# Kernel tuning notes

Measured on AMD Instinct MI355X. Metric: run time of the kernel, lower is better.

Reference implementation:

```python
import jax, jax.numpy as jnp
import numpy as np

B, N_PER, F_IN, HID, DEG = 64, 1024, 64, 128, 16
N = B * N_PER
E = N * DEG

def _ceil_k(k):
    return -((-4 * k) // 5)  # ceil(0.8 * k), static python int

def setup_inputs():
    key = jax.random.key(0)
    ks = jax.random.split(key, 16)
    x = jax.random.normal(ks[0], (N, F_IN), jnp.float32)
    # edges are intra-graph: local endpoints in [0, N_PER) offset by graph id
    loc = jax.random.randint(ks[1], (2, E), 0, N_PER, jnp.int32)
    gid = jnp.repeat(jnp.arange(B, dtype=jnp.int32), E // B)
    edge_index = loc + gid[None, :] * N_PER
    batch = jnp.repeat(jnp.arange(B, dtype=jnp.int32), N_PER)
    def lin(k, fi, fo):
        s = 1.0 / float(np.sqrt(fi))
        return jax.random.uniform(k, (fi, fo), jnp.float32, -s, s)
    inp = dict(x=x, edge_index=edge_index, batch=batch)
    inp["Wr1"] = lin(ks[2], F_IN, HID); inp["Wn1"] = lin(ks[3], F_IN, HID); inp["b1"] = jnp.zeros((HID,), jnp.float32)
    inp["Wr2"] = lin(ks[4], HID, HID); inp["Wn2"] = lin(ks[5], HID, HID); inp["b2"] = jnp.zeros((HID,), jnp.float32)
    inp["Wr3"] = lin(ks[6], HID, HID); inp["Wn3"] = lin(ks[7], HID, HID); inp["b3"] = jnp.zeros((HID,), jnp.float32)
    inp["p1"] = jax.random.normal(ks[8], (HID,), jnp.float32)
    inp["p2"] = jax.random.normal(ks[9], (HID,), jnp.float32)
    inp["p3"] = jax.random.normal(ks[10], (HID,), jnp.float32)
    inp["l1w"] = lin(ks[11], 2 * HID, HID); inp["l1b"] = jnp.zeros((HID,), jnp.float32)
    inp["l2w"] = lin(ks[12], HID, 2); inp["l2b"] = jnp.zeros((2,), jnp.float32)
    return inp

def _graph_conv(x, src, dst, emask, Wr, Wn, b, n_nodes):
    # x'_i = W1 x_i + sum_{j->i} W2 x_j + b ; masked edges contribute 0
    msg = x[src] * emask[:, None]                                  # [E, H]
    agg = jax.ops.segment_sum(msg, dst, num_segments=n_nodes)     # [N, H]
    return x @ Wr + agg @ Wn + b

def _topk_pool(x, src, dst, emask, p, k_prev):
    # PyG TopKPooling: score = x.p/||p||, keep ceil(0.8*n) per graph,
    # x_out = x[perm] * tanh(score[perm]); relabel+filter edges
    k_new = _ceil_k(k_prev)
    s = (x @ p) / jnp.linalg.norm(p)                               # [B*k_prev]
    vals, idx = jax.lax.top_k(s.reshape(B, k_prev), k_new)        # [B, k_new]
    perm = (idx + jnp.arange(B, dtype=idx.dtype)[:, None] * k_prev).reshape(-1)
    x_new = x[perm] * jnp.tanh(vals.reshape(-1))[:, None]
    inv = jnp.full((B * k_prev,), -1, jnp.int32).at[perm].set(jnp.arange(B * k_new, dtype=jnp.int32))
    ns, nd = inv[src], inv[dst]
    valid = emask * ((ns >= 0) & (nd >= 0)).astype(x.dtype)
    return x_new, jnp.maximum(ns, 0), jnp.maximum(nd, 0), valid, k_new

def _readout(x, k):
    b = jnp.repeat(jnp.arange(B, dtype=jnp.int32), k)
    gmax = jax.ops.segment_max(x, b, num_segments=B)
    gmean = jax.ops.segment_sum(x, b, num_segments=B) / k
    return jnp.concatenate([gmax, gmean], axis=1)                  # [B, 2H]

def reference(x, edge_index, batch, Wr1, Wn1, b1, Wr2, Wn2, b2, Wr3, Wn3, b3, p1, p2, p3, l1w, l1b, l2w, l2b):
    src, dst = edge_index[0], edge_index[1]
    emask = jnp.ones((E,), x.dtype)
    k = N_PER
    convs = [(Wr1, Wn1, b1), (Wr2, Wn2, b2), (Wr3, Wn3, b3)]
    pools = [p1, p2, p3]
    xs = []
    for (Wr, Wn, bb), p in zip(convs, pools):
        x = jax.nn.relu(_graph_conv(x, src, dst, emask, Wr, Wn, bb, B * k))
        x, src, dst, emask, k = _topk_pool(x, src, dst, emask, p, k)
        xs.append(_readout(x, k))
    h = xs[0] + xs[1] + xs[2]
    h = jax.nn.relu(h @ l1w + l1b)
    # F.dropout(p=0.5) skipped: eval-mode reference
    h = jax.nn.relu(h @ l2w + l2b)
    return jax.nn.log_softmax(h, axis=-1)
```

## Files before the change

kernel.cpp:

```cpp
#include <hip/hip_runtime.h>
#include <hip/hip_bf16.h>
#include <math.h>

#define NN   65536
#define NPER 1024
#define NE   1048576
#define NB   64

typedef __attribute__((ext_vector_type(8))) short short8;
typedef __attribute__((ext_vector_type(4))) float f32x4;


__global__ __launch_bounds__(256) void count_kernel(const int* __restrict__ ei, int* __restrict__ cnt){
  int e = blockIdx.x*256 + threadIdx.x;
  if (e < NE) atomicAdd(&cnt[ei[NE + e]], 1);
}

__global__ __launch_bounds__(1024) void scan1_kernel(const int* __restrict__ cnt,
      int* __restrict__ loc, int* __restrict__ bsum){
  __shared__ int wsum[16];
  int t = threadIdx.x;
  int i = blockIdx.x*1024 + t;
  int lane = t & 63, wid = t >> 6;
  int v = cnt[i];
  int s = v;
  #pragma unroll
  for (int d = 1; d < 64; d <<= 1){
    int src = (lane >= d) ? (lane - d) : lane;
    int u = __shfl(s, src);
    if (lane >= d) s += u;
  }
  if (lane == 63) wsum[wid] = s;
  __syncthreads();
  if (wid == 0){
    int ws = (lane < 16) ? wsum[lane] : 0;
    #pragma unroll
    for (int d = 1; d < 16; d <<= 1){
      int src = (lane >= d) ? (lane - d) : lane;
      int u = __shfl(ws, src);
      if (lane >= d) ws += u;
    }
    if (lane < 16) wsum[lane] = ws;
  }
  __syncthreads();
  int base = (wid > 0) ? wsum[wid - 1] : 0;
  loc[i] = base + s - v;
  if (t == 1023) bsum[blockIdx.x] = base + s;
}

__global__ __launch_bounds__(64) void scan2_kernel(const int* __restrict__ bsum, int* __restrict__ boff){
  int t = threadIdx.x;
  int v = bsum[t];
  int s = v;
  #pragma unroll
  for (int d = 1; d < 64; d <<= 1){
    int src = (t >= d) ? (t - d) : t;
    int u = __shfl(s, src);
    if (t >= d) s += u;
  }
  boff[t] = s - v;
}

__global__ __launch_bounds__(1024) void scan3_kernel(const int* __restrict__ loc, const int* __restrict__ boff,
      int* __restrict__ off, int* __restrict__ cursor){
  int i = blockIdx.x*1024 + threadIdx.x;
  int v = loc[i] + boff[blockIdx.x];
  off[i] = v;
  cursor[i] = v;
  if (i == NN - 1) off[NN] = NE;
}

__global__ __launch_bounds__(256) void fill_kernel(const int* __restrict__ ei, int* cursor, int* __restrict__ adj){
  int e = blockIdx.x*256 + threadIdx.x;
  if (e < NE){
    int pos = atomicAdd(&cursor[ei[NE + e]], 1);
    adj[pos] = ei[e];
  }
}


__global__ __launch_bounds__(256) void compact_kernel(const int* __restrict__ off, const int* __restrict__ adj,
      const float* __restrict__ scale, const int* __restrict__ alive,
      int* __restrict__ adj2, float* __restrict__ scl2, int* __restrict__ deg2){
  int w = (blockIdx.x*256 + (int)threadIdx.x) >> 6;
  int lane = threadIdx.x & 63;
  if (w >= NN) return;
  if (!alive[w]){ if (lane == 0) deg2[w] = 0; return; }
  int s0 = off[w], s1 = off[w+1];
  int base = s0;
  for (int e0 = s0; e0 < s1; e0 += 64){
    int e = e0 + lane;
    bool okE = e < s1;
    int s = adj[okE ? e : (s1 - 1)];
    float t = scale[s];
    bool keep = okE && (t != 0.f);
    unsigned long long m = __ballot(keep);
    int pos = base + __popcll(m & ((1ull << lane) - 1ull));
    if (keep){ adj2[pos] = s; scl2[pos] = t; }
    base += __popcll(m);
  }
  if (lane == 0) deg2[w] = base - s0;
}


__global__ __launch_bounds__(256) void gather_kernel(const float* __restrict__ x, int stride, int F,
      const int* __restrict__ off, const int* __restrict__ adj, const float* __restrict__ scl,
      const int* __restrict__ deg2, float* __restrict__ agg, const int* __restrict__ alive){
  int bid = blockIdx.x;
  bid = (bid & 7) * (gridDim.x >> 3) + (bid >> 3);
  int w = (bid*256 + (int)threadIdx.x) >> 6;
  int lane = threadIdx.x & 63;
  if (w >= NN) return;
  if (alive && !alive[w]) return;
  int s0 = off[w];
  int s1 = deg2 ? (s0 + deg2[w]) : off[w+1];
  if (F == 64){
    int sub = lane >> 4;
    int fl  = (lane & 15) * 4;
    float4 a0 = make_float4(0.f,0.f,0.f,0.f), a1 = a0;
    if (s1 > s0){
      for (int e = s0; e < s1; e += 8){
        int e0 = e + sub, e1 = e + 4 + sub;
        bool ok0 = e0 < s1, ok1 = e1 < s1;
        int sA = adj[ok0 ? e0 : (s1 - 1)];
        int sB = adj[ok1 ? e1 : (s1 - 1)];
        float t0 = ok0 ? 1.f : 0.f, t1 = ok1 ? 1.f : 0.f;
        float4 vA = *(const float4*)&x[(size_t)sA*stride + fl];
        float4 vB = *(const float4*)&x[(size_t)sB*stride + fl];
        a0.x = fmaf(vA.x, t0, a0.x); a0.y = fmaf(vA.y, t0, a0.y);
        a0.z = fmaf(vA.z, t0, a0.z); a0.w = fmaf(vA.w, t0, a0.w);
        a1.x = fmaf(vB.x, t1, a1.x); a1.y = fmaf(vB.y, t1, a1.y);
        a1.z = fmaf(vB.z, t1, a1.z); a1.w = fmaf(vB.w, t1, a1.w);
      }
    }
    a0.x += a1.x; a0.y += a1.y; a0.z += a1.z; a0.w += a1.w;
    #pragma unroll
    for (int m = 16; m <= 32; m <<= 1){
      a0.x += __shfl_xor(a0.x, m);
      a0.y += __shfl_xor(a0.y, m);
      a0.z += __shfl_xor(a0.z, m);
      a0.w += __shfl_xor(a0.w, m);
    }
    if (lane < 16) *(float4*)&agg[(size_t)w*128 + fl] = a0;
  } else {
    int sub = lane >> 5;
    int fl  = (lane & 31) * 4;
    float4 a[4];
    #pragma unroll
    for (int i = 0; i < 4; ++i) a[i] = make_float4(0.f,0.f,0.f,0.f);
    if (s1 > s0){
      for (int e = s0; e < s1; e += 8){
        int ss[4]; float tv[4];
        #pragma unroll
        for (int i = 0; i < 4; ++i){
          int ei = e + 2*i + sub;
          bool okE = ei < s1;
          int ii = okE ? ei : (s1 - 1);
          ss[i] = adj[ii];
          tv[i] = okE ? scl[ii] : 0.f;
        }
        #pragma unroll
        for (int i = 0; i < 4; ++i){
          float4 v = *(const float4*)&x[(size_t)ss[i]*stride + fl];
          a[i].x = fmaf(v.x, tv[i], a[i].x);
          a[i].y = fmaf(v.y, tv[i], a[i].y);
          a[i].z = fmaf(v.z, tv[i], a[i].z);
          a[i].w = fmaf(v.w, tv[i], a[i].w);
        }
      }
    }
    float4 r;
    r.x = (a[0].x + a[1].x) + (a[2].x + a[3].x);
    r.y = (a[0].y + a[1].y) + (a[2].y + a[3].y);
    r.z = (a[0].z + a[1].z) + (a[2].z + a[3].z);
    r.w = (a[0].w + a[1].w) + (a[2].w + a[3].w);
    r.x += __shfl_xor(r.x, 32);
    r.y += __shfl_xor(r.y, 32);
    r.z += __shfl_xor(r.z, 32);
    r.w += __shfl_xor(r.w, 32);
    if (lane < 32) *(float4*)&agg[(size_t)w*128 + fl] = r;
  }
}


__global__ __launch_bounds__(256) void wsplit_kernel(const float* __restrict__ Wr, const float* __restrict__ Wn,
      int Kx, int Kcat, unsigned short* __restrict__ WTh, unsigned short* __restrict__ WTl){
  int idx = blockIdx.x*256 + threadIdx.x;
  if (idx >= Kcat*128) return;
  int c = idx & 127, k = idx >> 7;
  float w = (k < Kx) ? Wr[k*128 + c] : Wn[(k - Kx)*128 + c];
  __hip_bfloat16 h = __float2bfloat16(w);
  float hf = __bfloat162float(h);
  __hip_bfloat16 l = __float2bfloat16(w - hf);
  WTh[(size_t)c*Kcat + k] = reinterpret_cast<unsigned short&>(h);
  WTl[(size_t)c*Kcat + k] = reinterpret_cast<unsigned short&>(l);
}


__global__ __launch_bounds__(256, 2) void conv_kernel(const float* __restrict__ xsrc, int strideX, int ntx,
      const float* aggb, int nta,
      const unsigned short* __restrict__ WTh, const unsigned short* __restrict__ WTl, int Kcat,
      const float* __restrict__ bias, const float* __restrict__ p, const float* __restrict__ scaleX,
      float* yout, float* __restrict__ score){
  __shared__ unsigned short XhL[128*32], XlL[128*32];
  __shared__ unsigned short WhL[128*32], WlL[128*32];
  __shared__ float sbuf[128*2];
  const int tid = threadIdx.x;
  const int row0 = blockIdx.x * 128;
  const int srow = tid & 127;
  const int shalf = tid >> 7;
  const int lane = tid & 63;
  const int wid = tid >> 6;
  const int wr = wid >> 1, wc = wid & 1;
  const int l15 = lane & 15, lkq = lane >> 4;

  const float xscale = scaleX ? scaleX[row0 + srow] : 1.f;

  f32x4 acc[4][4];
  #pragma unroll
  for (int m = 0; m < 4; ++m)
    #pragma unroll
    for (int j = 0; j < 4; ++j)
      acc[m][j] = (f32x4){0.f, 0.f, 0.f, 0.f};

  const int nt = ntx + nta;
  for (int t = 0; t < nt; ++t){
    __syncthreads();
    {
      const float* Xs   = (t < ntx) ? xsrc : aggb;
      const int stride  = (t < ntx) ? strideX : 128;
      const int kc      = (t < ntx) ? t*32 : (t - ntx)*32;
      const float sc    = (t < ntx) ? xscale : 1.f;
      #pragma unroll
      for (int kq2 = 0; kq2 < 2; ++kq2){
        const int kq = shalf*2 + kq2;
        const float* xp = Xs + (size_t)(row0 + srow)*stride + kc + kq*8;
        float4 v0 = *(const float4*)(xp);
        float4 v1 = *(const float4*)(xp + 4);
        float vv[8] = {v0.x*sc, v0.y*sc, v0.z*sc, v0.w*sc,
                       v1.x*sc, v1.y*sc, v1.z*sc, v1.w*sc};
        short8 hs, ls;
        #pragma unroll
        for (int q = 0; q < 8; ++q){
          __hip_bfloat16 h = __float2bfloat16(vv[q]);
          float hf = __bfloat162float(h);
          __hip_bfloat16 lo = __float2bfloat16(vv[q] - hf);
          hs[q] = reinterpret_cast<short&>(h);
          ls[q] = reinterpret_cast<short&>(lo);
        }
        const int kqph = kq ^ (srow & 3);
        *(short8*)&XhL[srow*32 + kqph*8] = hs;
        *(short8*)&XlL[srow*32 + kqph*8] = ls;
      }
      const int kcw = t*32;
      #pragma unroll
      for (int kq2 = 0; kq2 < 2; ++kq2){
        const int kq = shalf*2 + kq2;
        short8 h = *(const short8*)&WTh[(size_t)srow*Kcat + kcw + kq*8];
        short8 l = *(const short8*)&WTl[(size_t)srow*Kcat + kcw + kq*8];
        const int kqph = kq ^ (srow & 3);
        *(short8*)&WhL[srow*32 + kqph*8] = h;
        *(short8*)&WlL[srow*32 + kqph*8] = l;
      }
    }
    __syncthreads();
    short8 bh[4], bl[4];
    #pragma unroll
    for (int j = 0; j < 4; ++j){
      const int col = wc*64 + j*16 + l15;
      const int offb = col*32 + (lkq ^ (col & 3))*8;
      bh[j] = *(const short8*)&WhL[offb];
      bl[j] = *(const short8*)&WlL[offb];
    }
    #pragma unroll
    for (int m = 0; m < 4; ++m){
      const int row = wr*64 + m*16 + l15;
      const int offa = row*32 + (lkq ^ (row & 3))*8;
      short8 ah = *(const short8*)&XhL[offa];
      short8 al = *(const short8*)&XlL[offa];
      #pragma unroll
      for (int j = 0; j < 4; ++j){
        acc[m][j] = __builtin_amdgcn_mfma_f32_16x16x32_bf16(ah, bh[j], acc[m][j], 0, 0, 0);
        acc[m][j] = __builtin_amdgcn_mfma_f32_16x16x32_bf16(ah, bl[j], acc[m][j], 0, 0, 0);
        acc[m][j] = __builtin_amdgcn_mfma_f32_16x16x32_bf16(al, bh[j], acc[m][j], 0, 0, 0);
      }
    }
  }

  #pragma unroll
  for (int m = 0; m < 4; ++m){
    float prt[4] = {0.f, 0.f, 0.f, 0.f};
    #pragma unroll
    for (int j = 0; j < 4; ++j){
      const int col = wc*64 + j*16 + l15;
      const float bcol = bias[col];
      const float pcol = p[col];
      f32x4 a = acc[m][j];
      #pragma unroll
      for (int r = 0; r < 4; ++r){
        const int row = wr*64 + m*16 + lkq*4 + r;
        float y = fmaxf(a[r] + bcol, 0.f);
        yout[(size_t)(row0 + row)*128 + col] = y;
        prt[r] = fmaf(y, pcol, prt[r]);
      }
    }
    #pragma unroll
    for (int r = 0; r < 4; ++r){
      #pragma unroll
      for (int msk = 8; msk >= 1; msk >>= 1) prt[r] += __shfl_xor(prt[r], msk);
      if (l15 == 0) sbuf[(wr*64 + m*16 + lkq*4 + r)*2 + wc] = prt[r];
    }
  }
  __syncthreads();
  if (tid < 128) score[row0 + tid] = sbuf[tid*2] + sbuf[tid*2 + 1];
}


__global__ __launch_bounds__(1024) void topk_kernel(const float* __restrict__ score, const int* __restrict__ alive_cur,
      int* __restrict__ alive_next, float* __restrict__ scale, const float* __restrict__ p, int m){
  __shared__ float lv[1024];
  __shared__ int   li[1024];
  __shared__ float rnorm;
  const int g = blockIdx.x, t = threadIdx.x;
  if (t < 64){
    float v0 = p[t], v1 = p[t + 64];
    float ss = v0*v0 + v1*v1;
    #pragma unroll
    for (int mm = 32; mm >= 1; mm >>= 1) ss += __shfl_xor(ss, mm);
    if (t == 0) rnorm = rsqrtf(ss);
  }
  const int node = g*NPER + t;
  bool ok = alive_cur ? (alive_cur[node] != 0) : true;
  float v = ok ? score[node] : -INFINITY;
  int idx = node;
  alive_next[node] = 0;
  scale[node] = 0.f;

  auto cex_shfl = [&](int stride, bool dirUp){
    float vj = __shfl_xor(v, stride);
    int   ij = __shfl_xor(idx, stride);
    bool iAmLow = (t & stride) == 0;
    bool mineFirst = (v > vj) || (v == vj && idx < ij);
    bool takeMine = ((dirUp == iAmLow) == mineFirst);
    v   = takeMine ? v   : vj;
    idx = takeMine ? idx : ij;
  };
  auto cex_lds = [&](int stride, bool dirUp){
    __syncthreads();
    lv[t] = v; li[t] = idx;
    __syncthreads();
    float vj = lv[t ^ stride];
    int   ij = li[t ^ stride];
    bool iAmLow = (t & stride) == 0;
    bool mineFirst = (v > vj) || (v == vj && idx < ij);
    bool takeMine = ((dirUp == iAmLow) == mineFirst);
    v   = takeMine ? v   : vj;
    idx = takeMine ? idx : ij;
  };

  #pragma unroll
  for (int size = 2; size <= 64; size <<= 1){
    const bool dirUp = (t & size) == 0;
    for (int stride = size >> 1; stride >= 1; stride >>= 1)
      cex_shfl(stride, dirUp);
  }
  #pragma unroll
  for (int size = 128; size <= 1024; size <<= 1){
    const bool dirUp = (t & size) == 0;
    for (int stride = size >> 1; stride >= 64; stride >>= 1)
      cex_lds(stride, dirUp);
    for (int stride = 32; stride >= 1; stride >>= 1)
      cex_shfl(stride, dirUp);
  }

  if (t < m){
    alive_next[idx] = 1;
    scale[idx] = tanhf(v * rnorm);
  }
}


__global__ __launch_bounds__(1024) void readout_kernel(const float* __restrict__ y,
      const int* __restrict__ alive, const float* __restrict__ scale,
      float* __restrict__ h, int m){
  __shared__ float smx[64][17];
  __shared__ float ssm[64][17];
  int g = blockIdx.x;
  int fq = blockIdx.y;
  int t = threadIdx.x;
  int c  = t >> 4;
  int lf = t & 15;
  int f  = fq*16 + lf;
  int base = g*NPER;
  float mx[4] = {-INFINITY, -INFINITY, -INFINITY, -INFINITY};
  float sm[4] = {0.f, 0.f, 0.f, 0.f};
  #pragma unroll
  for (int i = 0; i < 16; i += 4){
    #pragma unroll
    for (int q = 0; q < 4; ++q){
      int node = base + c + (i + q)*64;
      int al = alive[node];
      float o = y[(size_t)node*128 + f] * scale[node];
      mx[q] = al ? fmaxf(mx[q], o) : mx[q];
      sm[q] += o;
    }
  }
  float mxa = fmaxf(fmaxf(mx[0], mx[1]), fmaxf(mx[2], mx[3]));
  float sma = (sm[0] + sm[1]) + (sm[2] + sm[3]);
  smx[c][lf] = mxa; ssm[c][lf] = sma;
  __syncthreads();
  for (int s = 32; s > 0; s >>= 1){
    if (c < s){
      smx[c][lf] = fmaxf(smx[c][lf], smx[c+s][lf]);
      ssm[c][lf] += ssm[c+s][lf];
    }
    __syncthreads();
  }
  if (c == 0){
    h[g*256 + f]       += smx[0][lf];
    h[g*256 + 128 + f] += ssm[0][lf] / (float)m;
  }
}


__global__ __launch_bounds__(128) void final_kernel(const float* __restrict__ h,
      const float* __restrict__ l1w, const float* __restrict__ l1b,
      const float* __restrict__ l2w, const float* __restrict__ l2b,
      float* __restrict__ out){
  int g = blockIdx.x, t = threadIdx.x;
  __shared__ float hrow[256];
  __shared__ float red0[128], red1[128];
  hrow[t]       = h[g*256 + t];
  hrow[t + 128] = h[g*256 + 128 + t];
  __syncthreads();
  float a = l1b[t];
  for (int k = 0; k < 256; ++k) a = fmaf(hrow[k], l1w[k*128 + t], a);
  a = fmaxf(a, 0.f);
  red0[t] = a * l2w[t*2 + 0];
  red1[t] = a * l2w[t*2 + 1];
  __syncthreads();
  for (int s = 64; s > 0; s >>= 1){
    if (t < s){ red0[t] += red0[t + s]; red1[t] += red1[t + s]; }
    __syncthreads();
  }
  if (t == 0){
    float z0 = fmaxf(red0[0] + l2b[0], 0.f);
    float z1 = fmaxf(red1[0] + l2b[1], 0.f);
    float mz = fmaxf(z0, z1);
    float lse = mz + logf(expf(z0 - mz) + expf(z1 - mz));
    out[g*2 + 0] = z0 - lse;
    out[g*2 + 1] = z1 - lse;
  }
}


static inline size_t alignup(size_t x){ return (x + 255) & ~(size_t)255; }

extern "C" void kernel_launch(void* const* d_in, const int* in_sizes, int n_in,
                              void* d_out, int out_size, void* d_ws, size_t ws_size,
                              hipStream_t stream) {
  const float* x_in = (const float*)d_in[0];
  const int*   ei   = (const int*)d_in[1];
  const float* Wr[3] = {(const float*)d_in[3], (const float*)d_in[6], (const float*)d_in[9]};
  const float* Wn[3] = {(const float*)d_in[4], (const float*)d_in[7], (const float*)d_in[10]};
  const float* bs[3] = {(const float*)d_in[5], (const float*)d_in[8], (const float*)d_in[11]};
  const float* ps[3] = {(const float*)d_in[12], (const float*)d_in[13], (const float*)d_in[14]};
  const float* l1w = (const float*)d_in[15];
  const float* l1b = (const float*)d_in[16];
  const float* l2w = (const float*)d_in[17];
  const float* l2b = (const float*)d_in[18];
  float* out = (float*)d_out;

  char* w = (char*)d_ws;
  size_t o = 0;
  auto take = [&](size_t bytes) -> void* { void* p = w + o; o = alignup(o + bytes); return p; };
  int*   off    = (int*)  take((size_t)(NN + 1) * 4);
  int*   adj    = (int*)  take((size_t)NE * 4);
  int*   adj2   = (int*)  take((size_t)NE * 4);
  float* scl2   = (float*)take((size_t)NE * 4);
  int*   deg2   = (int*)  take((size_t)NN * 4);
  int*   cnt    = (int*)  take((size_t)NN * 4);
  int*   loc    = (int*)  take((size_t)NN * 4);
  int*   cursor = (int*)  take((size_t)NN * 4);
  int*   bsum   = (int*)  take(64 * 4);
  int*   boff   = (int*)  take(64 * 4);
  int*   aliveA = (int*)  take((size_t)NN * 4);
  int*   aliveB = (int*)  take((size_t)NN * 4);
  float* scale  = (float*)take((size_t)NN * 4);
  float* score  = (float*)take((size_t)NN * 4);
  float* h      = (float*)take((size_t)NB * 256 * 4);
  unsigned short* WTh = (unsigned short*)take((size_t)128 * 256 * 2);
  unsigned short* WTl = (unsigned short*)take((size_t)128 * 256 * 2);
  float* A      = (float*)take((size_t)NN * 128 * 4);
  float* Bb     = (float*)take((size_t)NN * 128 * 4);
  (void)ws_size; (void)n_in; (void)in_sizes; (void)out_size;

  hipMemsetAsync(cnt, 0, (size_t)NN * 4, stream);
  count_kernel<<<NE/256, 256, 0, stream>>>(ei, cnt);
  scan1_kernel<<<NN/1024, 1024, 0, stream>>>(cnt, loc, bsum);
  scan2_kernel<<<1, 64, 0, stream>>>(bsum, boff);
  scan3_kernel<<<NN/1024, 1024, 0, stream>>>(loc, boff, off, cursor);
  fill_kernel<<<NE/256, 256, 0, stream>>>(ei, cursor, adj);
  hipMemsetAsync(h, 0, (size_t)NB * 256 * 4, stream);

  const int MS[3] = {820, 656, 525};
  int* aliveCur = nullptr;
  int* aliveNext = aliveA;
  float* bufs[2] = {Bb, A};
  for (int l = 0; l < 3; ++l){
    const int Kx = (l == 0) ? 64 : 128;
    const int Ka = (l == 0) ? 64 : 128;
    const int Kcat = Kx + Ka;
    float* aggb = bufs[l & 1];
    wsplit_kernel<<<(Kcat*128 + 255)/256, 256, 0, stream>>>(Wr[l], Wn[l], Kx, Kcat, WTh, WTl);
    if (l == 0){
      gather_kernel<<<NN*64/256, 256, 0, stream>>>(x_in, 64, 64, off, adj, nullptr, nullptr, aggb, nullptr);
      conv_kernel<<<NN/128, 256, 0, stream>>>(x_in, 64, Kx/32, aggb, Ka/32, WTh, WTl, Kcat,
                                              bs[0], ps[0], nullptr, aggb, score);
    } else {
      const float* ysrc = bufs[(l - 1) & 1];
      compact_kernel<<<NN*64/256, 256, 0, stream>>>(off, adj, scale, aliveCur, adj2, scl2, deg2);
      gather_kernel<<<NN*64/256, 256, 0, stream>>>(ysrc, 128, 128, off, adj2, scl2, deg2, aggb, aliveCur);
      conv_kernel<<<NN/128, 256, 0, stream>>>(ysrc, 128, Kx/32, aggb, Ka/32, WTh, WTl, Kcat,
                                              bs[l], ps[l], scale, aggb, score);
    }
    topk_kernel<<<NB, 1024, 0, stream>>>(score, aliveCur, aliveNext, scale, ps[l], MS[l]);
    readout_kernel<<<dim3(NB, 8), 1024, 0, stream>>>(aggb, aliveNext, scale, h, MS[l]);
    aliveCur = aliveNext;
    aliveNext = (l == 0) ? aliveB : aliveA;
  }
  final_kernel<<<NB, 128, 0, stream>>>(h, l1w, l1b, l2w, l2b, out);
}
```

Measured before the change: 317.0 us.

## Merge weight splits into one launch, pre-shift gather offsets, use 1024-thread blocks

Replaces the three per-layer weight-split launches with one kernel that writes every layer's bf16 hi/lo transposed weights into separate regions before the loop. The compact kernel now stores neighbour indices pre-shifted into byte offsets, so the gather kernel adds them to a per-lane base pointer and skips the per-edge multiply. Gather and compact move from 256- to 1024-thread blocks with one wave per node, and the bounds checks are dropped because the node count divides evenly. The gains are fewer launches and slightly cheaper address arithmetic. The risks are different occupancy from the larger blocks and a byte offset held in 32 bits, which fits at this node count.

```diff
diff --git a/kernel.cpp b/kernel.cpp
--- a/kernel.cpp
+++ b/kernel.cpp
@@ -79,12 +79,11 @@
 }
 
 
-__global__ __launch_bounds__(256) void compact_kernel(const int* __restrict__ off, const int* __restrict__ adj,
+__global__ __launch_bounds__(1024) void compact_kernel(const int* __restrict__ off, const int* __restrict__ adj,
       const float* __restrict__ scale, const int* __restrict__ alive,
       int* __restrict__ adj2, float* __restrict__ scl2, int* __restrict__ deg2){
-  int w = (blockIdx.x*256 + (int)threadIdx.x) >> 6;
+  int w = blockIdx.x*16 + ((int)threadIdx.x >> 6);
   int lane = threadIdx.x & 63;
-  if (w >= NN) return;
   if (!alive[w]){ if (lane == 0) deg2[w] = 0; return; }
   int s0 = off[w], s1 = off[w+1];
   int base = s0;
@@ -96,37 +95,36 @@
     bool keep = okE && (t != 0.f);
     unsigned long long m = __ballot(keep);
     int pos = base + __popcll(m & ((1ull << lane) - 1ull));
-    if (keep){ adj2[pos] = s; scl2[pos] = t; }
+    if (keep){ adj2[pos] = s << 9; scl2[pos] = t; }
     base += __popcll(m);
   }
   if (lane == 0) deg2[w] = base - s0;
 }
 
 
-__global__ __launch_bounds__(256) void gather_kernel(const float* __restrict__ x, int stride, int F,
-      const int* __restrict__ off, const int* __restrict__ adj, const float* __restrict__ scl,
+__global__ __launch_bounds__(1024) void gather_kernel(const float* __restrict__ x, int F,
+      const int* __restrict__ off, const int* __restrict__ adjB, const float* __restrict__ scl,
       const int* __restrict__ deg2, float* __restrict__ agg, const int* __restrict__ alive){
   int bid = blockIdx.x;
   bid = (bid & 7) * (gridDim.x >> 3) + (bid >> 3);
-  int w = (bid*256 + (int)threadIdx.x) >> 6;
+  int w = bid*16 + ((int)threadIdx.x >> 6);
   int lane = threadIdx.x & 63;
-  if (w >= NN) return;
   if (alive && !alive[w]) return;
   int s0 = off[w];
   int s1 = deg2 ? (s0 + deg2[w]) : off[w+1];
   if (F == 64){
+    const char* xb = (const char*)x + (lane & 15)*16;
     int sub = lane >> 4;
-    int fl  = (lane & 15) * 4;
     float4 a0 = make_float4(0.f,0.f,0.f,0.f), a1 = a0;
     if (s1 > s0){
       for (int e = s0; e < s1; e += 8){
         int e0 = e + sub, e1 = e + 4 + sub;
         bool ok0 = e0 < s1, ok1 = e1 < s1;
-        int sA = adj[ok0 ? e0 : (s1 - 1)];
-        int sB = adj[ok1 ? e1 : (s1 - 1)];
+        size_t oA = (size_t)(unsigned)adjB[ok0 ? e0 : (s1 - 1)] << 8;
+        size_t oB = (size_t)(unsigned)adjB[ok1 ? e1 : (s1 - 1)] << 8;
         float t0 = ok0 ? 1.f : 0.f, t1 = ok1 ? 1.f : 0.f;
-        float4 vA = *(const float4*)&x[(size_t)sA*stride + fl];
-        float4 vB = *(const float4*)&x[(size_t)sB*stride + fl];
+        float4 vA = *(const float4*)(xb + oA);
+        float4 vB = *(const float4*)(xb + oB);
         a0.x = fmaf(vA.x, t0, a0.x); a0.y = fmaf(vA.y, t0, a0.y);
         a0.z = fmaf(vA.z, t0, a0.z); a0.w = fmaf(vA.w, t0, a0.w);
         a1.x = fmaf(vB.x, t1, a1.x); a1.y = fmaf(vB.y, t1, a1.y);
@@ -141,10 +139,10 @@
       a0.z += __shfl_xor(a0.z, m);
       a0.w += __shfl_xor(a0.w, m);
     }
-    if (lane < 16) *(float4*)&agg[(size_t)w*128 + fl] = a0;
+    if (lane < 16) *(float4*)&agg[(size_t)w*128 + (lane & 15)*4] = a0;
   } else {
+    const char* xb = (const char*)x + (lane & 31)*16;
     int sub = lane >> 5;
-    int fl  = (lane & 31) * 4;
     float4 a[4];
     #pragma unroll
     for (int i = 0; i < 4; ++i) a[i] = make_float4(0.f,0.f,0.f,0.f);
@@ -156,12 +154,12 @@
           int ei = e + 2*i + sub;
           bool okE = ei < s1;
           int ii = okE ? ei : (s1 - 1);
-          ss[i] = adj[ii];
+          ss[i] = adjB[ii];
           tv[i] = okE ? scl[ii] : 0.f;
         }
         #pragma unroll
         for (int i = 0; i < 4; ++i){
-          float4 v = *(const float4*)&x[(size_t)ss[i]*stride + fl];
+          float4 v = *(const float4*)(xb + (size_t)(unsigned)ss[i]);
           a[i].x = fmaf(v.x, tv[i], a[i].x);
           a[i].y = fmaf(v.y, tv[i], a[i].y);
           a[i].z = fmaf(v.z, tv[i], a[i].z);
@@ -178,22 +176,29 @@
     r.y += __shfl_xor(r.y, 32);
     r.z += __shfl_xor(r.z, 32);
     r.w += __shfl_xor(r.w, 32);
-    if (lane < 32) *(float4*)&agg[(size_t)w*128 + fl] = r;
-  }
-}
-
-
-__global__ __launch_bounds__(256) void wsplit_kernel(const float* __restrict__ Wr, const float* __restrict__ Wn,
-      int Kx, int Kcat, unsigned short* __restrict__ WTh, unsigned short* __restrict__ WTl){
+    if (lane < 32) *(float4*)&agg[(size_t)w*128 + (lane & 31)*4] = r;
+  }
+}
+
+
+__global__ __launch_bounds__(256) void wsplit_all_kernel(
+      const float* __restrict__ Wr0, const float* __restrict__ Wn0,
+      const float* __restrict__ Wr1, const float* __restrict__ Wn1,
+      const float* __restrict__ Wr2, const float* __restrict__ Wn2,
+      unsigned short* __restrict__ WTh, unsigned short* __restrict__ WTl){
   int idx = blockIdx.x*256 + threadIdx.x;
-  if (idx >= Kcat*128) return;
-  int c = idx & 127, k = idx >> 7;
+  int rel, Kcat, Kx, base;
+  const float *Wr, *Wn;
+  if (idx < 16384){ rel = idx;          Kcat = 128; Kx = 64;  base = 0;     Wr = Wr0; Wn = Wn0; }
+  else if (idx < 49152){ rel = idx - 16384; Kcat = 256; Kx = 128; base = 16384; Wr = Wr1; Wn = Wn1; }
+  else { rel = idx - 49152; Kcat = 256; Kx = 128; base = 49152; Wr = Wr2; Wn = Wn2; }
+  int c = rel & 127, k = rel >> 7;
   float w = (k < Kx) ? Wr[k*128 + c] : Wn[(k - Kx)*128 + c];
   __hip_bfloat16 h = __float2bfloat16(w);
   float hf = __bfloat162float(h);
   __hip_bfloat16 l = __float2bfloat16(w - hf);
-  WTh[(size_t)c*Kcat + k] = reinterpret_cast<unsigned short&>(h);
-  WTl[(size_t)c*Kcat + k] = reinterpret_cast<unsigned short&>(l);
+  WTh[base + c*Kcat + k] = reinterpret_cast<unsigned short&>(h);
+  WTl[base + c*Kcat + k] = reinterpret_cast<unsigned short&>(l);
 }
 
 
@@ -489,8 +494,8 @@
   float* scale  = (float*)take((size_t)NN * 4);
   float* score  = (float*)take((size_t)NN * 4);
   float* h      = (float*)take((size_t)NB * 256 * 4);
-  unsigned short* WTh = (unsigned short*)take((size_t)128 * 256 * 2);
-  unsigned short* WTl = (unsigned short*)take((size_t)128 * 256 * 2);
+  unsigned short* WTh = (unsigned short*)take((size_t)81920 * 2);
+  unsigned short* WTl = (unsigned short*)take((size_t)81920 * 2);
   float* A      = (float*)take((size_t)NN * 128 * 4);
   float* Bb     = (float*)take((size_t)NN * 128 * 4);
   (void)ws_size; (void)n_in; (void)in_sizes; (void)out_size;
@@ -502,26 +507,27 @@
   scan3_kernel<<<NN/1024, 1024, 0, stream>>>(loc, boff, off, cursor);
   fill_kernel<<<NE/256, 256, 0, stream>>>(ei, cursor, adj);
   hipMemsetAsync(h, 0, (size_t)NB * 256 * 4, stream);
-
-  const int MS[3] = {820, 656, 525};
+  wsplit_all_kernel<<<320, 256, 0, stream>>>(Wr[0], Wn[0], Wr[1], Wn[1], Wr[2], Wn[2], WTh, WTl);
+
+  const int MS[3]   = {820, 656, 525};
+  const int WOFF[3] = {0, 16384, 49152};
+  const int KCAT[3] = {128, 256, 256};
   int* aliveCur = nullptr;
   int* aliveNext = aliveA;
   float* bufs[2] = {Bb, A};
   for (int l = 0; l < 3; ++l){
     const int Kx = (l == 0) ? 64 : 128;
     const int Ka = (l == 0) ? 64 : 128;
-    const int Kcat = Kx + Ka;
     float* aggb = bufs[l & 1];
-    wsplit_kernel<<<(Kcat*128 + 255)/256, 256, 0, stream>>>(Wr[l], Wn[l], Kx, Kcat, WTh, WTl);
     if (l == 0){
-      gather_kernel<<<NN*64/256, 256, 0, stream>>>(x_in, 64, 64, off, adj, nullptr, nullptr, aggb, nullptr);
-      conv_kernel<<<NN/128, 256, 0, stream>>>(x_in, 64, Kx/32, aggb, Ka/32, WTh, WTl, Kcat,
+      gather_kernel<<<NN/16, 1024, 0, stream>>>(x_in, 64, off, adj, nullptr, nullptr, aggb, nullptr);
+      conv_kernel<<<NN/128, 256, 0, stream>>>(x_in, 64, Kx/32, aggb, Ka/32, WTh + WOFF[0], WTl + WOFF[0], KCAT[0],
                                               bs[0], ps[0], nullptr, aggb, score);
     } else {
       const float* ysrc = bufs[(l - 1) & 1];
-      compact_kernel<<<NN*64/256, 256, 0, stream>>>(off, adj, scale, aliveCur, adj2, scl2, deg2);
-      gather_kernel<<<NN*64/256, 256, 0, stream>>>(ysrc, 128, 128, off, adj2, scl2, deg2, aggb, aliveCur);
-      conv_kernel<<<NN/128, 256, 0, stream>>>(ysrc, 128, Kx/32, aggb, Ka/32, WTh, WTl, Kcat,
+      compact_kernel<<<NN/16, 1024, 0, stream>>>(off, adj, scale, aliveCur, adj2, scl2, deg2);
+      gather_kernel<<<NN/16, 1024, 0, stream>>>(ysrc, 128, off, adj2, scl2, deg2, aggb, aliveCur);
+      conv_kernel<<<NN/128, 256, 0, stream>>>(ysrc, 128, Kx/32, aggb, Ka/32, WTh + WOFF[l], WTl + WOFF[l], KCAT[l],
                                               bs[l], ps[l], scale, aggb, score);
     }
     topk_kernel<<<NB, 1024, 0, stream>>>(score, aliveCur, aliveNext, scale, ps[l], MS[l]);
```

Measured after the change: 325.8 us. 1.03x slower.
